# Kernel optimization log

Hardware: AMD Instinct MI355X
Metric: run time of the kernel (lower is better)

Reference implementation:

```python
import jax, jax.numpy as jnp
import numpy as np

# dims: batch, tokens, channels, heads, head_dim, slices, context_slices, context_dim
B, N, C, H, D, G, SC, DC = 2, 32768, 256, 8, 32, 32, 64, 32
EPS_SLICE = 1e-5


def _ln(x, g, b):
    m = x.mean(-1, keepdims=True)
    v = ((x - m) ** 2).mean(-1, keepdims=True)
    return (x - m) * jax.lax.rsqrt(v + 1e-5) * g + b


def setup_inputs() -> dict:
    key = jax.random.key(0)
    ks = jax.random.split(key, 16)
    w = lambda k, s: jax.random.normal(k, s, jnp.float32) * 0.02
    return dict(
        fx=jax.random.normal(ks[0], (B, N, C), jnp.float32),
        context=jax.random.normal(ks[1], (B, H, SC, DC), jnp.float32),
        ln1_g=jnp.ones((C,), jnp.float32), ln1_b=jnp.zeros((C,), jnp.float32),
        Wfx=w(ks[2], (C, H * D)), bfx=jnp.zeros((H * D,), jnp.float32),
        Wx=w(ks[3], (C, H * D)), bx=jnp.zeros((H * D,), jnp.float32),
        Wslice=w(ks[4], (D, G)), bslice=jnp.zeros((G,), jnp.float32),
        temperature=0.5 * jnp.ones((1, H, 1, 1), jnp.float32),
        Wq=w(ks[5], (D, D)), Wk=w(ks[6], (D, D)), Wv=w(ks[7], (D, D)),
        Wcq=w(ks[8], (D, D)), bcq=jnp.zeros((D,), jnp.float32),
        Wck=w(ks[9], (DC, D)), bck=jnp.zeros((D,), jnp.float32),
        Wcv=w(ks[10], (DC, D)), bcv=jnp.zeros((D,), jnp.float32),
        state_mixing=jnp.zeros((), jnp.float32),
        Wout=w(ks[11], (H * D, C)), bout=jnp.zeros((C,), jnp.float32),
        ln2_g=jnp.ones((C,), jnp.float32), ln2_b=jnp.zeros((C,), jnp.float32),
        Wm1=w(ks[12], (C, 4 * C)), bm1=jnp.zeros((4 * C,), jnp.float32),
        Wm2=w(ks[13], (4 * C, C)), bm2=jnp.zeros((C,), jnp.float32),
    )


def reference(fx, context, ln1_g, ln1_b, Wfx, bfx, Wx, bx, Wslice, bslice,
              temperature, Wq, Wk, Wv, Wcq, bcq, Wck, bck, Wcv, bcv,
              state_mixing, Wout, bout, ln2_g, ln2_b, Wm1, bm1, Wm2, bm2):
    # --- GALE attention on pre-normed input (Transolver physics attention + cross) ---
    x = _ln(fx, ln1_g, ln1_b)
    fxm = (x @ Wfx + bfx).reshape(B, N, H, D).transpose(0, 2, 1, 3)  # b h n d
    xm = (x @ Wx + bx).reshape(B, N, H, D).transpose(0, 2, 1, 3)    # b h n d
    # slice weights: softmax over slices with learnable per-head temperature
    sw = jax.nn.softmax((xm @ Wslice + bslice) / temperature, axis=-1)  # b h n g
    norm = sw.sum(2)  # b h g
    st = jnp.einsum('bhnd,bhng->bhgd', fxm, sw) / (norm + EPS_SLICE)[..., None]
    scale = D ** -0.5
    # self-attention among slice tokens (no bias on q/k/v)
    q, k, v = st @ Wq, st @ Wk, st @ Wv
    sattn = jax.nn.softmax(jnp.einsum('bhgd,bhmd->bhgm', q, k) * scale, axis=-1)
    self_tok = jnp.einsum('bhgm,bhmd->bhgd', sattn, v)
    # cross-attention of slice tokens onto geometry/global context
    cq = st @ Wcq + bcq
    ck = context @ Wck + bck
    cv = context @ Wcv + bcv
    cattn = jax.nn.softmax(jnp.einsum('bhgd,bhsd->bhgs', cq, ck) * scale, axis=-1)
    cross_tok = jnp.einsum('bhgs,bhsd->bhgd', cattn, cv)
    # sigmoid-gated mix
    mw = jax.nn.sigmoid(state_mixing)
    ost = mw * self_tok + (1.0 - mw) * cross_tok
    # de-slice back to tokens and output-project
    out = jnp.einsum('bhgd,bhng->bhnd', ost, sw)
    out = out.transpose(0, 2, 1, 3).reshape(B, N, H * D) @ Wout + bout
    fx = fx + out  # residual 1
    # --- MLP block ---
    h = _ln(fx, ln2_g, ln2_b)
    fx = fx + (jax.nn.gelu(h @ Wm1 + bm1, approximate=False) @ Wm2 + bm2)
    return fx
```

## Files before the change

### kernel.cpp

```cpp
#include <hip/hip_runtime.h>
#include <hip/hip_bf16.h>

#define BATCH 2
#define NTOK  32768
#define CH    256
#define NH    8
#define HDIM  32
#define NG    32
#define NSC   64
#define NDC   32

typedef __attribute__((ext_vector_type(8))) short short8v;
typedef __attribute__((ext_vector_type(4))) short short4v;
typedef __attribute__((ext_vector_type(4))) float f32x4;

static __device__ __forceinline__ short f2bf(float f) {
    __hip_bfloat16 h = __float2bfloat16(f);
    return __builtin_bit_cast(short, h);
}
static __device__ __forceinline__ float bf2f(short s) {
    return __bfloat162float(__builtin_bit_cast(__hip_bfloat16, s));
}

__global__ __launch_bounds__(256) void kconv_transpose(
    const float* __restrict__ in, __hip_bfloat16* __restrict__ out,
    int K, int N)
{
    __shared__ float t[32][33];
    const int nb = N >> 5;
    const int bk = blockIdx.x / nb;
    const int bn = blockIdx.x % nb;
    const int c = threadIdx.x & 31, r0 = threadIdx.x >> 5;
    #pragma unroll
    for (int i = 0; i < 4; ++i) {
        const int r = r0 + i * 8;
        t[r][c] = in[(long)(bk * 32 + r) * N + bn * 32 + c];
    }
    __syncthreads();
    #pragma unroll
    for (int i = 0; i < 4; ++i) {
        const int r = r0 + i * 8;
        out[(long)(bn * 32 + r) * K + bk * 32 + c] = __float2bfloat16(t[c][r]);
    }
}

__global__ __launch_bounds__(256) void kcomb(
    const float* __restrict__ Wx, const float* __restrict__ bx,
    const float* __restrict__ Wsl, const float* __restrict__ bsl,
    __hip_bfloat16* __restrict__ wcat2, float* __restrict__ bcomb)
{
    __shared__ float wcol[32];
    const int hc = blockIdx.x;
    const int h = hc >> 5, g = hc & 31;
    const int tid = threadIdx.x;
    if (tid < 32) wcol[tid] = Wsl[tid * 32 + g];
    __syncthreads();
    float a = 0.f;
    #pragma unroll
    for (int d = 0; d < 32; ++d) a += Wx[tid * 256 + h * 32 + d] * wcol[d];
    wcat2[(long)hc * 256 + tid] = __float2bfloat16(a);
    if (tid == 0) {
        float s = bsl[g];
        #pragma unroll
        for (int d = 0; d < 32; ++d) s += bx[h * 32 + d] * wcol[d];
        bcomb[hc] = s;
    }
}

__global__ __launch_bounds__(256, 2) void k1_mfma(
    const float* __restrict__ fx,
    const float* __restrict__ g1, const float* __restrict__ b1,
    const __hip_bfloat16* __restrict__ wcat,
    const float* __restrict__ bfx, const float* __restrict__ bcomb,
    const float* __restrict__ temp,
    __hip_bfloat16* __restrict__ fxm_o, __hip_bfloat16* __restrict__ sw_o)
{
    __shared__ __align__(16) char lds[65536];
    const int tid = threadIdx.x;
    const int lane = tid & 63, wid = tid >> 6;
    const long tok0 = (long)blockIdx.x * 64;
    const int col = lane & 15, kq = lane >> 4;
    const int swz = (col & 7) << 4;
    const int ep = ((kq * 16) ^ swz) & 48;
    const int e0 = (swz & 64) | ep;
    const int e1 = ((swz & 64) ^ 64) | ep;
    const int ab0 = col * 512 + e0, ab1 = col * 512 + e1;

    {
        const float4 gv = *reinterpret_cast<const float4*>(g1 + lane * 4);
        const float4 bv = *reinterpret_cast<const float4*>(b1 + lane * 4);
        for (int tt = 0; tt < 16; ++tt) {
            const int r = wid * 16 + tt;
            const float4 v = *reinterpret_cast<const float4*>(fx + (tok0 + r) * 256 + lane * 4);
            float s = v.x + v.y + v.z + v.w;
            float s2 = v.x * v.x + v.y * v.y + v.z * v.z + v.w * v.w;
            #pragma unroll
            for (int off = 32; off; off >>= 1) {
                s  += __shfl_xor(s,  off);
                s2 += __shfl_xor(s2, off);
            }
            const float mean = s * (1.f / 256.f);
            const float rs = rsqrtf(s2 * (1.f / 256.f) - mean * mean + 1e-5f);
            short4v o;
            o[0] = f2bf((v.x - mean) * rs * gv.x + bv.x);
            o[1] = f2bf((v.y - mean) * rs * gv.y + bv.y);
            o[2] = f2bf((v.z - mean) * rs * gv.z + bv.z);
            o[3] = f2bf((v.w - mean) * rs * gv.w + bv.w);
            const int addr = r * 512 + ((lane * 8) ^ ((r & 7) << 4));
            *reinterpret_cast<short4v*>(lds + addr) = o;
        }
    }
    __syncthreads();

    f32x4 acc[4][8];
    #pragma unroll
    for (int mt = 0; mt < 4; ++mt)
        #pragma unroll
        for (int nt = 0; nt < 8; ++nt) acc[mt][nt] = (f32x4){0.f, 0.f, 0.f, 0.f};

    const short* wp = reinterpret_cast<const short*>(wcat) + (wid * 128 + col) * 256 + kq * 8;
    #pragma unroll 2
    for (int j = 0; j < 4; ++j) {
        short8v a0[4], a1[4];
        #pragma unroll
        for (int mt = 0; mt < 4; ++mt) {
            a0[mt] = *reinterpret_cast<const short8v*>(lds + mt * 8192 + j * 128 + ab0);
            a1[mt] = *reinterpret_cast<const short8v*>(lds + mt * 8192 + j * 128 + ab1);
        }
        #pragma unroll
        for (int nt = 0; nt < 8; ++nt) {
            const short8v b0 = *reinterpret_cast<const short8v*>(wp + nt * 4096 + j * 64);
            const short8v b1 = *reinterpret_cast<const short8v*>(wp + nt * 4096 + j * 64 + 32);
            #pragma unroll
            for (int mt = 0; mt < 4; ++mt) {
                acc[mt][nt] = __builtin_amdgcn_mfma_f32_16x16x32_bf16(a0[mt], b0, acc[mt][nt], 0, 0, 0);
                acc[mt][nt] = __builtin_amdgcn_mfma_f32_16x16x32_bf16(a1[mt], b1, acc[mt][nt], 0, 0, 0);
            }
        }
    }
    __syncthreads();

    #pragma unroll
    for (int nt = 0; nt < 8; ++nt) {
        const int c = wid * 128 + nt * 16 + col;
        const float bb = (c < 256) ? bfx[c] : bcomb[c - 256];
        #pragma unroll
        for (int mt = 0; mt < 4; ++mt) {
            #pragma unroll
            for (int r = 0; r < 4; ++r) {
                const int row = mt * 16 + kq * 4 + r;
                const int byte = row * 1024 + ((c * 2) ^ ((row & 7) << 4));
                *reinterpret_cast<short*>(lds + byte) = f2bf(acc[mt][nt][r] + bb);
            }
        }
    }
    __syncthreads();

    #pragma unroll
    for (int it = 0; it < 8; ++it) {
        const int idx = it * 256 + tid;
        const int row = idx >> 5, ch = idx & 31;
        const short8v val = *reinterpret_cast<const short8v*>(
            lds + row * 1024 + ((ch * 16) ^ ((row & 7) << 4)));
        *reinterpret_cast<short8v*>(
            reinterpret_cast<short*>(fxm_o) + (tok0 + row) * 256 + ch * 8) = val;
    }

    #pragma unroll
    for (int pp = 0; pp < 2; ++pp) {
        const int p = pp * 256 + tid;
        const int t = p >> 3, h = p & 7;
        const float it_ = 1.f / temp[h];
        float lg[32];
        #pragma unroll
        for (int g = 0; g < 32; ++g) {
            const int byte = t * 1024 + (((256 + h * 32 + g) * 2) ^ ((t & 7) << 4));
            lg[g] = bf2f(*reinterpret_cast<const short*>(lds + byte)) * it_;
        }
        float mx = -1e30f;
        #pragma unroll
        for (int g = 0; g < 32; ++g) mx = fmaxf(mx, lg[g]);
        float ssum = 0.f;
        #pragma unroll
        for (int g = 0; g < 32; ++g) { lg[g] = __expf(lg[g] - mx); ssum += lg[g]; }
        const float inv = 1.f / ssum;
        #pragma unroll
        for (int g = 0; g < 32; ++g) {
            const int byte = t * 1024 + (((256 + h * 32 + g) * 2) ^ ((t & 7) << 4));
            *reinterpret_cast<short*>(lds + byte) = f2bf(lg[g] * inv);
        }
    }
    __syncthreads();

    #pragma unroll
    for (int it = 0; it < 8; ++it) {
        const int idx = it * 256 + tid;
        const int row = idx >> 5, ch = idx & 31;
        const short8v val = *reinterpret_cast<const short8v*>(
            lds + row * 1024 + ((512 + ch * 16) ^ ((row & 7) << 4)));
        *reinterpret_cast<short8v*>(
            reinterpret_cast<short*>(sw_o) + (tok0 + row) * 256 + ch * 8) = val;
    }
}

__global__ __launch_bounds__(512) void k2_st_partial(
    const __hip_bfloat16* __restrict__ fxm, const __hip_bfloat16* __restrict__ sw,
    float* __restrict__ pst, float* __restrict__ pn)
{
    __shared__ float psum[8][32][32];
    __shared__ float pns[8][32];
    const int tid = threadIdx.x, wid = tid >> 6, lane = tid & 63;
    const int blk = blockIdx.x;
    const int bh = blk >> 5, chunk = blk & 31;
    const int b = bh >> 3, h = bh & 7;
    const long rbase = (long)b * NTOK + (long)chunk * 1024 + wid * 128;
    const int gB = lane >> 3, dB = lane & 7;
    const short* sp = reinterpret_cast<const short*>(sw) + rbase * 256 + h * 32 + gB * 4;
    const short* fp = reinterpret_cast<const short*>(fxm) + rbase * 256 + h * 32 + dB * 4;

    float acc[4][4];
    float nacc[4];
    #pragma unroll
    for (int i = 0; i < 4; ++i) {
        nacc[i] = 0.f;
        #pragma unroll
        for (int j = 0; j < 4; ++j) acc[i][j] = 0.f;
    }

    #pragma unroll 4
    for (int r = 0; r < 128; ++r) {
        const short4v s4 = *reinterpret_cast<const short4v*>(sp + r * 256);
        const short4v f4 = *reinterpret_cast<const short4v*>(fp + r * 256);
        float sg[4], fd[4];
        #pragma unroll
        for (int i = 0; i < 4; ++i) { sg[i] = bf2f(s4[i]); fd[i] = bf2f(f4[i]); }
        #pragma unroll
        for (int gg = 0; gg < 4; ++gg) {
            nacc[gg] += sg[gg];
            #pragma unroll
            for (int dd = 0; dd < 4; ++dd) acc[gg][dd] += sg[gg] * fd[dd];
        }
    }

    #pragma unroll
    for (int gg = 0; gg < 4; ++gg) {
        #pragma unroll
        for (int dd = 0; dd < 4; ++dd)
            psum[wid][gB * 4 + gg][dB * 4 + dd] = acc[gg][dd];
        if (dB == 0) pns[wid][gB * 4 + gg] = nacc[gg];
    }
    __syncthreads();

    for (int i = tid; i < 1024; i += 512) {
        const int g = i >> 5, d = i & 31;
        float s = 0.f;
        #pragma unroll
        for (int w = 0; w < 8; ++w) s += psum[w][g][d];
        pst[(long)blk * 1024 + i] = s;
    }
    if (tid < 32) {
        float s = 0.f;
        #pragma unroll
        for (int w = 0; w < 8; ++w) s += pns[w][tid];
        pn[blk * 32 + tid] = s;
    }
}

__global__ __launch_bounds__(256) void k3_slice_attn(
    const float* __restrict__ pst, const float* __restrict__ pn,
    const float* __restrict__ ctx,
    const float* __restrict__ Wq, const float* __restrict__ Wk, const float* __restrict__ Wv,
    const float* __restrict__ Wcq, const float* __restrict__ bcq,
    const float* __restrict__ Wck, const float* __restrict__ bck,
    const float* __restrict__ Wcv, const float* __restrict__ bcv,
    const float* __restrict__ mix, __hip_bfloat16* __restrict__ ostT_o)
{
    __shared__ float st[1024], qm[1024], km[1024], vm[1024], cqm[1024];
    __shared__ float ckm[2048], cvm[2048], attn[2048], stok[1024], nb[32];
    const int tid = threadIdx.x;
    const int bh = blockIdx.x;

    if (tid < 32) {
        float s = 0.f;
        for (int c = 0; c < 32; ++c) s += pn[(bh * 32 + c) * 32 + tid];
        nb[tid] = s;
    }
    __syncthreads();
    for (int i = tid; i < 1024; i += 256) {
        float s = 0.f;
        for (int c = 0; c < 32; ++c) s += pst[(long)(bh * 32 + c) * 1024 + i];
        st[i] = s / (nb[i >> 5] + 1e-5f);
    }
    __syncthreads();

    for (int i = tid; i < 1024; i += 256) {
        const int g = i >> 5, d = i & 31;
        float aq = 0.f, ak = 0.f, av = 0.f, ac = bcq[d];
        #pragma unroll
        for (int e = 0; e < 32; ++e) {
            const float s = st[g * 32 + e];
            aq += s * Wq[e * 32 + d];
            ak += s * Wk[e * 32 + d];
            av += s * Wv[e * 32 + d];
            ac += s * Wcq[e * 32 + d];
        }
        qm[i] = aq; km[i] = ak; vm[i] = av; cqm[i] = ac;
    }
    const float* cbp = ctx + (long)bh * (NSC * NDC);
    for (int i = tid; i < 2048; i += 256) {
        const int s_ = i >> 5, d = i & 31;
        float w1 = bck[d], w2 = bcv[d];
        #pragma unroll
        for (int e = 0; e < 32; ++e) {
            const float cval = cbp[s_ * 32 + e];
            w1 += cval * Wck[e * 32 + d];
            w2 += cval * Wcv[e * 32 + d];
        }
        ckm[i] = w1; cvm[i] = w2;
    }
    __syncthreads();

    const float scale = 0.17677669529663687f;
    for (int i = tid; i < 1024; i += 256) {
        const int g = i >> 5, m = i & 31;
        float a = 0.f;
        #pragma unroll
        for (int d = 0; d < 32; ++d) a += qm[g * 32 + d] * km[m * 32 + d];
        attn[i] = a * scale;
    }
    __syncthreads();
    if (tid < 32) {
        float mx = -1e30f;
        for (int m = 0; m < 32; ++m) mx = fmaxf(mx, attn[tid * 32 + m]);
        float s = 0.f;
        for (int m = 0; m < 32; ++m) { const float e = expf(attn[tid * 32 + m] - mx); attn[tid * 32 + m] = e; s += e; }
        const float inv = 1.f / s;
        for (int m = 0; m < 32; ++m) attn[tid * 32 + m] *= inv;
    }
    __syncthreads();
    for (int i = tid; i < 1024; i += 256) {
        const int g = i >> 5, d = i & 31;
        float a = 0.f;
        #pragma unroll
        for (int m = 0; m < 32; ++m) a += attn[g * 32 + m] * vm[m * 32 + d];
        stok[i] = a;
    }
    __syncthreads();
    for (int i = tid; i < 2048; i += 256) {
        const int g = i >> 6, s_ = i & 63;
        float a = 0.f;
        #pragma unroll
        for (int d = 0; d < 32; ++d) a += cqm[g * 32 + d] * ckm[s_ * 32 + d];
        attn[i] = a * scale;
    }
    __syncthreads();
    if (tid < 32) {
        float mx = -1e30f;
        for (int m = 0; m < 64; ++m) mx = fmaxf(mx, attn[tid * 64 + m]);
        float s = 0.f;
        for (int m = 0; m < 64; ++m) { const float e = expf(attn[tid * 64 + m] - mx); attn[tid * 64 + m] = e; s += e; }
        const float inv = 1.f / s;
        for (int m = 0; m < 64; ++m) attn[tid * 64 + m] *= inv;
    }
    __syncthreads();
    const float mw = 1.f / (1.f + expf(-mix[0]));
    for (int i = tid; i < 1024; i += 256) {
        const int g = i >> 5, d = i & 31;
        float a = 0.f;
        #pragma unroll
        for (int s_ = 0; s_ < 64; ++s_) a += attn[g * 64 + s_] * cvm[s_ * 32 + d];
        const float val = mw * stok[i] + (1.f - mw) * a;
        ostT_o[(long)bh * 1024 + d * 32 + g] = __float2bfloat16(val);
    }
}

__global__ __launch_bounds__(512, 4) void k45_fused(
    const __hip_bfloat16* __restrict__ sw, const __hip_bfloat16* __restrict__ ostT,
    const __hip_bfloat16* __restrict__ woutt, const float* __restrict__ bout,
    const float* __restrict__ fx,
    const float* __restrict__ g2, const float* __restrict__ b2,
    const __hip_bfloat16* __restrict__ w1t, const float* __restrict__ bm1,
    const __hip_bfloat16* __restrict__ w2t, const float* __restrict__ bm2,
    float* __restrict__ out)
{
    __shared__ __align__(16) char lds[65536];
    const int tid = threadIdx.x;
    const int lane = tid & 63, wid = tid >> 6;
    const long tok0 = (long)blockIdx.x * 64;
    const int b = (int)(tok0 >> 15);
    const int col = lane & 15, kq = lane >> 4;
    const int swz = (col & 7) << 4;
    const int ep = ((kq * 16) ^ swz) & 48;
    const int e0 = (swz & 64) | ep;
    const int e1 = ((swz & 64) ^ 64) | ep;
    const int ab0 = col * 512 + e0, ab1 = col * 512 + e1;

    #pragma unroll
    for (int it = 0; it < 4; ++it) {
        const int idx = it * 512 + tid;
        const int row = idx >> 5, ch = idx & 31;
        const short8v val = *reinterpret_cast<const short8v*>(
            reinterpret_cast<const short*>(sw) + (tok0 + row) * 256 + ch * 8);
        *reinterpret_cast<short8v*>(lds + row * 512 + ((ch * 16) ^ ((row & 7) << 4))) = val;
    }
    __syncthreads();

    {
        f32x4 accal[4][2];
        const int abh = col * 512 + (((wid * 64) | (kq * 16)) ^ swz);
        short8v a[4];
        #pragma unroll
        for (int mt = 0; mt < 4; ++mt)
            a[mt] = *reinterpret_cast<const short8v*>(lds + mt * 8192 + abh);
        #pragma unroll
        for (int nt = 0; nt < 2; ++nt) {
            const int d = nt * 16 + col;
            const short8v bfr = *reinterpret_cast<const short8v*>(
                reinterpret_cast<const short*>(ostT) + ((b * 8 + wid) * 32 + d) * 32 + kq * 8);
            #pragma unroll
            for (int mt = 0; mt < 4; ++mt) {
                accal[mt][nt] = (f32x4){0.f, 0.f, 0.f, 0.f};
                accal[mt][nt] = __builtin_amdgcn_mfma_f32_16x16x32_bf16(
                    a[mt], bfr, accal[mt][nt], 0, 0, 0);
            }
        }
        #pragma unroll
        for (int nt = 0; nt < 2; ++nt) {
            const int cc = wid * 32 + nt * 16 + col;
            #pragma unroll
            for (int mt = 0; mt < 4; ++mt) {
                #pragma unroll
                for (int r = 0; r < 4; ++r) {
                    const int row = mt * 16 + kq * 4 + r;
                    const int byte = 32768 + row * 512 + ((cc * 2) ^ ((row & 7) << 4));
                    *reinterpret_cast<short*>(lds + byte) = f2bf(accal[mt][nt][r]);
                }
            }
        }
    }
    __syncthreads();

    f32x4 acc[4][2];
    #pragma unroll
    for (int mt = 0; mt < 4; ++mt)
        #pragma unroll
        for (int nt = 0; nt < 2; ++nt) acc[mt][nt] = (f32x4){0.f, 0.f, 0.f, 0.f};

    {
        const short* wp = reinterpret_cast<const short*>(woutt) + (wid * 32 + col) * 256 + kq * 8;
        #pragma unroll 2
        for (int j = 0; j < 4; ++j) {
            short8v a0[4], a1[4];
            #pragma unroll
            for (int mt = 0; mt < 4; ++mt) {
                a0[mt] = *reinterpret_cast<const short8v*>(lds + 32768 + mt * 8192 + j * 128 + ab0);
                a1[mt] = *reinterpret_cast<const short8v*>(lds + 32768 + mt * 8192 + j * 128 + ab1);
            }
            #pragma unroll
            for (int nt = 0; nt < 2; ++nt) {
                const short8v b0 = *reinterpret_cast<const short8v*>(wp + nt * 4096 + j * 64);
                const short8v b1 = *reinterpret_cast<const short8v*>(wp + nt * 4096 + j * 64 + 32);
                #pragma unroll
                for (int mt = 0; mt < 4; ++mt) {
                    acc[mt][nt] = __builtin_amdgcn_mfma_f32_16x16x32_bf16(a0[mt], b0, acc[mt][nt], 0, 0, 0);
                    acc[mt][nt] = __builtin_amdgcn_mfma_f32_16x16x32_bf16(a1[mt], b1, acc[mt][nt], 0, 0, 0);
                }
            }
        }
    }

    __syncthreads();
    float* lf = reinterpret_cast<float*>(lds);
    #pragma unroll
    for (int nt = 0; nt < 2; ++nt) {
        const int c = wid * 32 + nt * 16 + col;
        const float bb = bout[c];
        #pragma unroll
        for (int mt = 0; mt < 4; ++mt) {
            #pragma unroll
            for (int r = 0; r < 4; ++r) {
                const int row = mt * 16 + kq * 4 + r;
                lf[row * 256 + c] = acc[mt][nt][r] + bb;
            }
        }
    }
    __syncthreads();

    short4v aout[8];
    {
        const float4 gv = *reinterpret_cast<const float4*>(g2 + lane * 4);
        const float4 bv = *reinterpret_cast<const float4*>(b2 + lane * 4);
        #pragma unroll
        for (int tt = 0; tt < 8; ++tt) {
            const int r = wid * 8 + tt;
            const float4 l4 = *reinterpret_cast<const float4*>(lf + r * 256 + lane * 4);
            const float4 f4 = *reinterpret_cast<const float4*>(fx + (tok0 + r) * 256 + lane * 4);
            float4 oa;
            oa.x = l4.x + f4.x; oa.y = l4.y + f4.y;
            oa.z = l4.z + f4.z; oa.w = l4.w + f4.w;
            *reinterpret_cast<float4*>(out + (tok0 + r) * 256 + lane * 4) = oa;
            float s = oa.x + oa.y + oa.z + oa.w;
            float s2 = oa.x * oa.x + oa.y * oa.y + oa.z * oa.z + oa.w * oa.w;
            #pragma unroll
            for (int off = 32; off; off >>= 1) {
                s  += __shfl_xor(s,  off);
                s2 += __shfl_xor(s2, off);
            }
            const float mean = s * (1.f / 256.f);
            const float rs = rsqrtf(s2 * (1.f / 256.f) - mean * mean + 1e-5f);
            aout[tt][0] = f2bf((oa.x - mean) * rs * gv.x + bv.x);
            aout[tt][1] = f2bf((oa.y - mean) * rs * gv.y + bv.y);
            aout[tt][2] = f2bf((oa.z - mean) * rs * gv.z + bv.z);
            aout[tt][3] = f2bf((oa.w - mean) * rs * gv.w + bv.w);
        }
    }
    __syncthreads();
    #pragma unroll
    for (int tt = 0; tt < 8; ++tt) {
        const int r = wid * 8 + tt;
        const int addr = r * 512 + ((lane * 8) ^ ((r & 7) << 4));
        *reinterpret_cast<short4v*>(lds + addr) = aout[tt];
    }
    __syncthreads();

    const int n0 = wid * 32;
    const short* w1s = reinterpret_cast<const short*>(w1t) + (n0 + col) * 256 + kq * 8;
    const short* w2s = reinterpret_cast<const short*>(w2t) + (n0 + col) * 1024 + kq * 8;
    const int gsw = (kq & 1) << 6;

    f32x4 accO[4][2];
    #pragma unroll
    for (int mt = 0; mt < 4; ++mt)
        #pragma unroll
        for (int nt = 0; nt < 2; ++nt) accO[mt][nt] = (f32x4){0.f, 0.f, 0.f, 0.f};

    for (int ch = 0; ch < 4; ++ch) {
        f32x4 accP[4][2];
        #pragma unroll
        for (int mt = 0; mt < 4; ++mt)
            #pragma unroll
            for (int nt = 0; nt < 2; ++nt) accP[mt][nt] = (f32x4){0.f, 0.f, 0.f, 0.f};

        #pragma unroll 2
        for (int j = 0; j < 4; ++j) {
            short8v a0[4], a1[4];
            #pragma unroll
            for (int mt = 0; mt < 4; ++mt) {
                a0[mt] = *reinterpret_cast<const short8v*>(lds + mt * 8192 + j * 128 + ab0);
                a1[mt] = *reinterpret_cast<const short8v*>(lds + mt * 8192 + j * 128 + ab1);
            }
            #pragma unroll
            for (int nt = 0; nt < 2; ++nt) {
                const short8v b0 = *reinterpret_cast<const short8v*>(
                    w1s + ch * 65536 + nt * 4096 + j * 64);
                const short8v b1 = *reinterpret_cast<const short8v*>(
                    w1s + ch * 65536 + nt * 4096 + j * 64 + 32);
                #pragma unroll
                for (int mt = 0; mt < 4; ++mt) {
                    accP[mt][nt] = __builtin_amdgcn_mfma_f32_16x16x32_bf16(a0[mt], b0, accP[mt][nt], 0, 0, 0);
                    accP[mt][nt] = __builtin_amdgcn_mfma_f32_16x16x32_bf16(a1[mt], b1, accP[mt][nt], 0, 0, 0);
                }
            }
        }

        __syncthreads();
        #pragma unroll
        for (int nt = 0; nt < 2; ++nt) {
            const float b1v = bm1[ch * 256 + n0 + nt * 16 + col];
            const int k2i2 = (n0 + nt * 16 + col) * 2;
            #pragma unroll
            for (int mt = 0; mt < 4; ++mt) {
                #pragma unroll
                for (int r = 0; r < 4; ++r) {
                    float m = accP[mt][nt][r] + b1v;
                    const float u = __builtin_fmaf(0.044715f * m, m * m, m);
                    const float e = __expf(-1.5957691216057308f * u);
                    m = m * __builtin_amdgcn_rcpf(1.f + e);
                    const int byte = 32768 + kq * 2048 + mt * 8192 + r * 512
                                     + (k2i2 ^ (gsw + r * 16));
                    *reinterpret_cast<short*>(lds + byte) = f2bf(m);
                }
            }
        }
        __syncthreads();

        #pragma unroll 2
        for (int j = 0; j < 4; ++j) {
            short8v a0[4], a1[4];
            #pragma unroll
            for (int mt = 0; mt < 4; ++mt) {
                a0[mt] = *reinterpret_cast<const short8v*>(lds + 32768 + mt * 8192 + j * 128 + ab0);
                a1[mt] = *reinterpret_cast<const short8v*>(lds + 32768 + mt * 8192 + j * 128 + ab1);
            }
            #pragma unroll
            for (int nt = 0; nt < 2; ++nt) {
                const short8v b0 = *reinterpret_cast<const short8v*>(
                    w2s + nt * 16384 + ch * 256 + j * 64);
                const short8v b1 = *reinterpret_cast<const short8v*>(
                    w2s + nt * 16384 + ch * 256 + j * 64 + 32);
                #pragma unroll
                for (int mt = 0; mt < 4; ++mt) {
                    accO[mt][nt] = __builtin_amdgcn_mfma_f32_16x16x32_bf16(a0[mt], b0, accO[mt][nt], 0, 0, 0);
                    accO[mt][nt] = __builtin_amdgcn_mfma_f32_16x16x32_bf16(a1[mt], b1, accO[mt][nt], 0, 0, 0);
                }
            }
        }
    }

    __syncthreads();
    #pragma unroll
    for (int nt = 0; nt < 2; ++nt) {
        const int c = n0 + nt * 16 + col;
        const float b2v = bm2[c];
        #pragma unroll
        for (int mt = 0; mt < 4; ++mt) {
            #pragma unroll
            for (int r = 0; r < 4; ++r) {
                const int row = mt * 16 + kq * 4 + r;
                lf[row * 256 + c] = accO[mt][nt][r] + b2v;
            }
        }
    }
    __syncthreads();
    #pragma unroll
    for (int tt = 0; tt < 8; ++tt) {
        const int r = wid * 8 + tt;
        const float4 m4 = *reinterpret_cast<const float4*>(lf + r * 256 + lane * 4);
        const long gidx = (tok0 + r) * 256 + lane * 4;
        const float4 oa = *reinterpret_cast<const float4*>(out + gidx);
        float4 o;
        o.x = oa.x + m4.x; o.y = oa.y + m4.y;
        o.z = oa.z + m4.z; o.w = oa.w + m4.w;
        *reinterpret_cast<float4*>(out + gidx) = o;
    }
}

extern "C" void kernel_launch(void* const* d_in, const int* in_sizes, int n_in,
                              void* d_out, int out_size, void* d_ws, size_t ws_size,
                              hipStream_t stream)
{
    const float* fx   = (const float*)d_in[0];
    const float* ctx  = (const float*)d_in[1];
    const float* g1   = (const float*)d_in[2];
    const float* b1   = (const float*)d_in[3];
    const float* Wfx  = (const float*)d_in[4];
    const float* bfx  = (const float*)d_in[5];
    const float* Wx   = (const float*)d_in[6];
    const float* bx   = (const float*)d_in[7];
    const float* Wsl  = (const float*)d_in[8];
    const float* bsl  = (const float*)d_in[9];
    const float* temp = (const float*)d_in[10];
    const float* Wq   = (const float*)d_in[11];
    const float* Wk   = (const float*)d_in[12];
    const float* Wv   = (const float*)d_in[13];
    const float* Wcq  = (const float*)d_in[14];
    const float* bcq  = (const float*)d_in[15];
    const float* Wck  = (const float*)d_in[16];
    const float* bck  = (const float*)d_in[17];
    const float* Wcv  = (const float*)d_in[18];
    const float* bcv  = (const float*)d_in[19];
    const float* mix  = (const float*)d_in[20];
    const float* Wout = (const float*)d_in[21];
    const float* bout = (const float*)d_in[22];
    const float* g2   = (const float*)d_in[23];
    const float* b2   = (const float*)d_in[24];
    const float* Wm1  = (const float*)d_in[25];
    const float* bm1  = (const float*)d_in[26];
    const float* Wm2  = (const float*)d_in[27];
    const float* bm2  = (const float*)d_in[28];
    float* out = (float*)d_out;

    char* ws = (char*)d_ws;
    __hip_bfloat16* fxm  = (__hip_bfloat16*)ws;
    __hip_bfloat16* sw   = (__hip_bfloat16*)(ws + (size_t)33554432);
    float* pst = (float*)(ws + (size_t)67108864);
    float* pn  = (float*)(ws + (size_t)69206016);
    __hip_bfloat16* ostT  = (__hip_bfloat16*)(ws + (size_t)69271552);
    __hip_bfloat16* wcat  = (__hip_bfloat16*)(ws + (size_t)69304320);
    __hip_bfloat16* woutt = (__hip_bfloat16*)(ws + (size_t)69566464);
    __hip_bfloat16* w1t   = (__hip_bfloat16*)(ws + (size_t)69697536);
    __hip_bfloat16* w2t   = (__hip_bfloat16*)(ws + (size_t)70221824);
    float* bcomb          = (float*)(ws + (size_t)70746112);

    kconv_transpose<<<64,  256, 0, stream>>>(Wfx, wcat,  256, 256);
    kcomb<<<256, 256, 0, stream>>>(Wx, bx, Wsl, bsl, wcat + 65536, bcomb);
    kconv_transpose<<<64,  256, 0, stream>>>(Wout, woutt, 256, 256);
    kconv_transpose<<<256, 256, 0, stream>>>(Wm1, w1t,    256, 1024);
    kconv_transpose<<<256, 256, 0, stream>>>(Wm2, w2t,    1024, 256);

    k1_mfma<<<1024, 256, 0, stream>>>(fx, g1, b1, wcat, bfx, bcomb, temp,
                                      fxm, sw);
    k2_st_partial<<<512, 512, 0, stream>>>(fxm, sw, pst, pn);
    k3_slice_attn<<<16, 256, 0, stream>>>(pst, pn, ctx, Wq, Wk, Wv,
                                          Wcq, bcq, Wck, bck, Wcv, bcv, mix, ostT);
    k45_fused<<<1024, 512, 0, stream>>>(sw, ostT, woutt, bout, fx,
                                        g2, b2, w1t, bm1, w2t, bm2, out);
}
```

Measured before the change: 325.0 us.

## Merge weight transpose launches and split k1 GEMM across eight waves

The four weight-transpose launches become one kernel that dispatches tiles by block index, which removes launch overhead. k1_mfma now runs 512 threads per block. Each of the eight waves computes 64 output columns instead of 128, and the layernorm, store and softmax loops are redistributed to match. This halves per-wave accumulator registers and raises wave-level parallelism within each 64-token tile, but it adds occupancy demands on the 64KB LDS per block.

Result: faster. 314.7 us (-3.2%).

```diff
diff --git a/kernel.cpp b/kernel.cpp
--- a/kernel.cpp
+++ b/kernel.cpp
@@ -22,15 +22,15 @@
     return __bfloat162float(__builtin_bit_cast(__hip_bfloat16, s));
 }
 
-__global__ __launch_bounds__(256) void kconv_transpose(
+static __device__ __forceinline__ void transpose_tile(
     const float* __restrict__ in, __hip_bfloat16* __restrict__ out,
-    int K, int N)
+    int K, int N, int blk, int tid)
 {
     __shared__ float t[32][33];
     const int nb = N >> 5;
-    const int bk = blockIdx.x / nb;
-    const int bn = blockIdx.x % nb;
-    const int c = threadIdx.x & 31, r0 = threadIdx.x >> 5;
+    const int bk = blk / nb;
+    const int bn = blk % nb;
+    const int c = tid & 31, r0 = tid >> 5;
     #pragma unroll
     for (int i = 0; i < 4; ++i) {
         const int r = r0 + i * 8;
@@ -42,6 +42,19 @@
         const int r = r0 + i * 8;
         out[(long)(bn * 32 + r) * K + bk * 32 + c] = __float2bfloat16(t[c][r]);
     }
+}
+
+__global__ __launch_bounds__(256) void kconv_all(
+    const float* __restrict__ Wfx, __hip_bfloat16* __restrict__ wcat,
+    const float* __restrict__ Wout, __hip_bfloat16* __restrict__ woutt,
+    const float* __restrict__ Wm1, __hip_bfloat16* __restrict__ w1t,
+    const float* __restrict__ Wm2, __hip_bfloat16* __restrict__ w2t)
+{
+    const int b = blockIdx.x, tid = threadIdx.x;
+    if (b < 64)            transpose_tile(Wfx,  wcat,  256, 256,  b,        tid);
+    else if (b < 128)      transpose_tile(Wout, woutt, 256, 256,  b - 64,   tid);
+    else if (b < 384)      transpose_tile(Wm1,  w1t,   256, 1024, b - 128,  tid);
+    else                   transpose_tile(Wm2,  w2t,   1024, 256, b - 384,  tid);
 }
 
 __global__ __launch_bounds__(256) void kcomb(
@@ -67,7 +80,7 @@
     }
 }
 
-__global__ __launch_bounds__(256, 2) void k1_mfma(
+__global__ __launch_bounds__(512, 4) void k1_mfma(
     const float* __restrict__ fx,
     const float* __restrict__ g1, const float* __restrict__ b1,
     const __hip_bfloat16* __restrict__ wcat,
@@ -89,8 +102,9 @@
     {
         const float4 gv = *reinterpret_cast<const float4*>(g1 + lane * 4);
         const float4 bv = *reinterpret_cast<const float4*>(b1 + lane * 4);
-        for (int tt = 0; tt < 16; ++tt) {
-            const int r = wid * 16 + tt;
+        #pragma unroll
+        for (int tt = 0; tt < 8; ++tt) {
+            const int r = wid * 8 + tt;
             const float4 v = *reinterpret_cast<const float4*>(fx + (tok0 + r) * 256 + lane * 4);
             float s = v.x + v.y + v.z + v.w;
             float s2 = v.x * v.x + v.y * v.y + v.z * v.z + v.w * v.w;
@@ -112,13 +126,14 @@
     }
     __syncthreads();
 
-    f32x4 acc[4][8];
+    const int n0 = wid * 64;
+    f32x4 acc[4][4];
     #pragma unroll
     for (int mt = 0; mt < 4; ++mt)
         #pragma unroll
-        for (int nt = 0; nt < 8; ++nt) acc[mt][nt] = (f32x4){0.f, 0.f, 0.f, 0.f};
-
-    const short* wp = reinterpret_cast<const short*>(wcat) + (wid * 128 + col) * 256 + kq * 8;
+        for (int nt = 0; nt < 4; ++nt) acc[mt][nt] = (f32x4){0.f, 0.f, 0.f, 0.f};
+
+    const short* wp = reinterpret_cast<const short*>(wcat) + (n0 + col) * 256 + kq * 8;
     #pragma unroll 2
     for (int j = 0; j < 4; ++j) {
         short8v a0[4], a1[4];
@@ -128,7 +143,7 @@
             a1[mt] = *reinterpret_cast<const short8v*>(lds + mt * 8192 + j * 128 + ab1);
         }
         #pragma unroll
-        for (int nt = 0; nt < 8; ++nt) {
+        for (int nt = 0; nt < 4; ++nt) {
             const short8v b0 = *reinterpret_cast<const short8v*>(wp + nt * 4096 + j * 64);
             const short8v b1 = *reinterpret_cast<const short8v*>(wp + nt * 4096 + j * 64 + 32);
             #pragma unroll
@@ -141,8 +156,8 @@
     __syncthreads();
 
     #pragma unroll
-    for (int nt = 0; nt < 8; ++nt) {
-        const int c = wid * 128 + nt * 16 + col;
+    for (int nt = 0; nt < 4; ++nt) {
+        const int c = n0 + nt * 16 + col;
         const float bb = (c < 256) ? bfx[c] : bcomb[c - 256];
         #pragma unroll
         for (int mt = 0; mt < 4; ++mt) {
@@ -157,8 +172,8 @@
     __syncthreads();
 
     #pragma unroll
-    for (int it = 0; it < 8; ++it) {
-        const int idx = it * 256 + tid;
+    for (int it = 0; it < 4; ++it) {
+        const int idx = it * 512 + tid;
         const int row = idx >> 5, ch = idx & 31;
         const short8v val = *reinterpret_cast<const short8v*>(
             lds + row * 1024 + ((ch * 16) ^ ((row & 7) << 4)));
@@ -166,10 +181,8 @@
             reinterpret_cast<short*>(fxm_o) + (tok0 + row) * 256 + ch * 8) = val;
     }
 
-    #pragma unroll
-    for (int pp = 0; pp < 2; ++pp) {
-        const int p = pp * 256 + tid;
-        const int t = p >> 3, h = p & 7;
+    {
+        const int t = tid >> 3, h = tid & 7;
         const float it_ = 1.f / temp[h];
         float lg[32];
         #pragma unroll
@@ -193,8 +206,8 @@
     __syncthreads();
 
     #pragma unroll
-    for (int it = 0; it < 8; ++it) {
-        const int idx = it * 256 + tid;
+    for (int it = 0; it < 4; ++it) {
+        const int idx = it * 512 + tid;
         const int row = idx >> 5, ch = idx & 31;
         const short8v val = *reinterpret_cast<const short8v*>(
             lds + row * 1024 + ((512 + ch * 16) ^ ((row & 7) << 4)));
@@ -682,13 +695,10 @@
     __hip_bfloat16* w2t   = (__hip_bfloat16*)(ws + (size_t)70221824);
     float* bcomb          = (float*)(ws + (size_t)70746112);
 
-    kconv_transpose<<<64,  256, 0, stream>>>(Wfx, wcat,  256, 256);
+    kconv_all<<<640, 256, 0, stream>>>(Wfx, wcat, Wout, woutt, Wm1, w1t, Wm2, w2t);
     kcomb<<<256, 256, 0, stream>>>(Wx, bx, Wsl, bsl, wcat + 65536, bcomb);
-    kconv_transpose<<<64,  256, 0, stream>>>(Wout, woutt, 256, 256);
-    kconv_transpose<<<256, 256, 0, stream>>>(Wm1, w1t,    256, 1024);
-    kconv_transpose<<<256, 256, 0, stream>>>(Wm2, w2t,    1024, 256);
-
-    k1_mfma<<<1024, 256, 0, stream>>>(fx, g1, b1, wcat, bfx, bcomb, temp,
+
+    k1_mfma<<<1024, 512, 0, stream>>>(fx, g1, b1, wcat, bfx, bcomb, temp,
                                       fxm, sw);
     k2_st_partial<<<512, 512, 0, stream>>>(fxm, sw, pst, pn);
     k3_slice_attn<<<16, 256, 0, stream>>>(pst, pn, ctx, Wq, Wk, Wv,
```
